# Optimization experiments

Measured on AMD Instinct MI355X. Metric: run time of the kernel, lower is better.

Reference implementation:

```python
import jax, jax.numpy as jnp
import numpy as np


def _gru_step(x, h, W_ih, W_hh, b_ih, b_hh):
    # torch GRUCell math, gate order (r, z, n)
    gx = x @ W_ih.T + b_ih
    gh = h @ W_hh.T + b_hh
    xr, xz, xn = jnp.split(gx, 3, axis=-1)
    hr, hz, hn = jnp.split(gh, 3, axis=-1)
    r = jax.nn.sigmoid(xr + hr)
    z = jax.nn.sigmoid(xz + hz)
    n = jnp.tanh(xn + r * hn)
    return (1.0 - z) * n + z * h


def setup_inputs() -> dict:
    T, B, S, E, H, Dv, EXT = 64, 16, 400, 128, 256, 50000, 50
    key = jax.random.key(0)
    ks = jax.random.split(key, 32)
    def rn(k, shape, s=0.05):
        return jax.random.normal(k, shape, dtype=jnp.float32) * s
    return {
        'embedded_y': rn(ks[0], (T, B, E), 1.0),
        'encode_outputs': rn(ks[1], (S, B, 2 * H), 1.0),
        'init_state': rn(ks[2], (B, H), 1.0),
        'x_mask': jnp.ones((S, B, 1), jnp.float32),
        'y_mask': jnp.ones((T, B, 1), jnp.float32),
        'x_index': jax.random.randint(ks[3], (S, B), 0, Dv + EXT),
        'max_ext_len': EXT,
        'init_coverage': jnp.zeros((B, S), jnp.float32),
        'W_h': rn(ks[4], (2 * H, 2 * H)),
        'W_s': rn(ks[5], (2 * H, H)),
        'W_c': rn(ks[6], (2 * H, 1)),
        'b_attn': rn(ks[7], (2 * H,)),
        'V_attn': rn(ks[8], (1, 2 * H)),
        'gru1_Wih': rn(ks[9], (3 * H, E)),
        'gru1_Whh': rn(ks[10], (3 * H, H)),
        'gru1_bih': rn(ks[11], (3 * H,)),
        'gru1_bhh': rn(ks[12], (3 * H,)),
        'gru2_Wih': rn(ks[13], (3 * H, 2 * H)),
        'gru2_Whh': rn(ks[14], (3 * H, H)),
        'gru2_bih': rn(ks[15], (3 * H,)),
        'gru2_bhh': rn(ks[16], (3 * H,)),
        'V1_w': rn(ks[17], (H, H + 2 * H + E)),
        'V1_b': rn(ks[18], (H,)),
        'V2_w': rn(ks[19], (Dv, H)),
        'V2_b': rn(ks[20], (Dv,)),
        'Wp_w': rn(ks[21], (1, H + 2 * H + E)),
        'Wp_b': rn(ks[22], (1,)),
    }


def reference(embedded_y, encode_outputs, init_state, x_mask, y_mask, x_index,
              max_ext_len, init_coverage, W_h, W_s, W_c, b_attn, V_attn,
              gru1_Wih, gru1_Whh, gru1_bih, gru1_bhh,
              gru2_Wih, gru2_Whh, gru2_bih, gru2_bhh,
              V1_w, V1_b, V2_w, V2_b, Wp_w, Wp_b):
    T, B, E = embedded_y.shape
    S = encode_outputs.shape[0]
    enc_proj = encode_outputs @ W_h.T  # [S,B,2H], time-invariant part of attention

    def step(carry, inp):
        hidden, cov = carry  # [B,H], [B,S]
        y_t, ym_t = inp      # [B,E], [B,1]
        s1 = _gru_step(y_t, hidden, gru1_Wih, gru1_Whh, gru1_bih, gru1_bhh)
        s1 = ym_t * s1 + (1.0 - ym_t) * hidden
        # coverage term: cov.T[:,:,None] is [S,B,1], Linear(1,2H)
        att = enc_proj + s1 @ W_s.T + cov.T[:, :, None] @ W_c.T + b_attn  # [S,B,2H]
        score = (jnp.tanh(att) * x_mask) @ V_attn.T                      # [S,B,1]
        score = jnp.where(x_mask == 0, -1e9, score)
        attn = jax.nn.softmax(score, axis=0)                             # over source len
        ctx = jnp.sum(attn * encode_outputs, axis=0)                     # [B,2H]
        s2 = _gru_step(ctx, s1, gru2_Wih, gru2_Whh, gru2_bih, gru2_bhh)
        s2 = ym_t * s2 + (1.0 - ym_t) * s1
        waw = attn[:, :, 0].T                                            # [B,S]
        return (s2, cov + waw), (s2, ctx, waw, cov)

    (_, _), (hs, cvs, waws, covs) = jax.lax.scan(
        step, (init_state, init_coverage), (embedded_y, y_mask))

    # WordProbLayer (pointer-generator)
    h = jnp.concatenate([hs, cvs, embedded_y], axis=2)         # [T,B,H+2H+E]
    logit = jnp.tanh(h @ V1_w.T + V1_b) @ V2_w.T + V2_b        # [T,B,Dv]
    y_dec = jax.nn.softmax(logit, axis=2)
    y_dec = jnp.concatenate(
        [y_dec, jnp.zeros((T, B, max_ext_len), y_dec.dtype)], axis=2)
    g = jax.nn.sigmoid(h @ Wp_w.T + Wp_b)                      # [T,B,1]
    xids = jnp.broadcast_to(x_index.T[None], (T, B, S))        # [T,B,S]
    ti = jnp.arange(T)[:, None, None]
    bi = jnp.arange(B)[None, :, None]
    y_pred = (g * y_dec).at[ti, bi, xids].add((1.0 - g) * waws)
    return (y_pred, hs, waws, covs)
```

## Files before the change

kernel.cpp:

```cpp
#include <hip/hip_runtime.h>
#include <hip/hip_bf16.h>

typedef unsigned short ushort_t;
typedef unsigned int u32;
typedef _Float16 f16;
typedef __attribute__((ext_vector_type(8))) short short8;
typedef __attribute__((ext_vector_type(4))) float f32x4;
typedef __attribute__((ext_vector_type(8))) _Float16 f16x8;
typedef __attribute__((ext_vector_type(4))) unsigned int u32x4;

#define T_ 64
#define B_ 16
#define S_ 400
#define E_ 128
#define H_ 256
#define H2_ 512
#define DV_ 50000
#define VOC_ 50050
#define CAT_ 896
#define NCLUS 8
#define RSL 50

#define YP_SZ   ((size_t)T_*B_*VOC_)
#define HS_OFF  (YP_SZ)
#define WW_OFF  (HS_OFF + (size_t)T_*B_*H_)
#define CV_OFF  (WW_OFF + (size_t)T_*B_*S_)
#define ENCP16_OFF ((size_t)0)
#define ENC16_OFF  ((size_t)1638400)
#define WS16_OFF   ((size_t)3276800)
#define W216_OFF   ((size_t)3342336)
#define CTXALL_OFF ((size_t)3538944)
#define GX1_OFF    ((size_t)4063232)
#define WH216_OFF  ((size_t)4947968)
#define WH116T_OFF ((size_t)5046272)
#define SYNC_OFF   ((size_t)5144576)
#define S1STR      528
#define S1TAG      520
#define S2STR      816
#define S2TAG      808
#define S2REG      ((size_t)16*NCLUS*S1STR)
#define SYNC_FLOATS ((size_t)16*NCLUS*(S1STR + S2STR))

#define WS_ROWSUM 0
#define WS_GV     1024
#define WS_G1     2048

__device__ __forceinline__ float fsig(float x){ return 1.f/(1.f+__expf(-x)); }
__device__ __forceinline__ float ftanh(float x){ float e=__expf(2.f*x); return 1.f - 2.f/(e+1.f); }

#define PADK(k) ((k) + (((k)>>5)<<2))

#define AT_ST(p, v)  __hip_atomic_store((p), (v), __ATOMIC_RELAXED, __HIP_MEMORY_SCOPE_AGENT)
#define AT_LD(p)     __hip_atomic_load((p), __ATOMIC_RELAXED, __HIP_MEMORY_SCOPE_AGENT)
#define AT_STI(p, v) __hip_atomic_store((int*)(p), (v), __ATOMIC_RELAXED, __HIP_MEMORY_SCOPE_AGENT)
#define AT_LDI(p)    __hip_atomic_load((const int*)(p), __ATOMIC_RELAXED, __HIP_MEMORY_SCOPE_AGENT)

#define SM_ENC    0
#define SM_ENCP   51200
#define SM_GH1    102400
#define SM_SWS    105472
#define SM_VP     107776
#define SM_WCP    110080
#define SM_UCTX   112384
#define SM_HID    114432
#define SM_S1     115456
#define SM_G2X    116480
#define SM_G2H    116864
#define SM_COV    117248
#define SM_EV     117504
#define SM_XM     117760
#define SM_YM     118016
#define SM_HIDH   118272
#define SM_S1H    118784
#define SM_CTXH   119296
#define SM_S2S    120320
#define SM_PART   120448
#define SM_B1     120512
#define SM_B2     123584
#define SM_B3     126656
#define SM_BYTES  129728

__global__ __launch_bounds__(256)
void cvt16_kernel(const float* src, f16* dst, int n){
  int i = blockIdx.x*256 + threadIdx.x;
  if (i < n) dst[i] = (f16)src[i];
}

__global__ __launch_bounds__(256)
void repack_kernel(const float* enc, f16* enc16){
  int s = blockIdx.x, b = blockIdx.y;
  const float* src = enc + ((size_t)s*B_ + b)*H2_;
  f16* dst = enc16 + ((size_t)b*S_ + s)*H2_;
  for (int k = threadIdx.x; k < H2_; k += 256) dst[k] = (f16)src[k];
}

__global__ __launch_bounds__(256)
void packWhh1_kernel(const float* W, f16* dst){
  int r = blockIdx.x, c = threadIdx.x;
  int jq = c >> 5, cc = c & 31;
  dst[((size_t)jq*768 + r)*32 + cc] = (f16)W[(size_t)r*H_ + c];
}

__global__ __launch_bounds__(256)
void gx1_kernel(const float* emb, const float* Wih1, const float* bih1, float* dout){
  __shared__ float As[64][33];
  __shared__ float Bs[128][33];
  int m0 = blockIdx.x*64, n0 = blockIdx.y*128;
  int tx = threadIdx.x & 15, ty = threadIdx.x >> 4;
  float acc[4][8] = {};
  for (int kt = 0; kt < E_; kt += 32){
    for (int l = threadIdx.x; l < 64*32; l += 256){
      int m = l>>5, k = l&31; As[m][k] = emb[(size_t)(m0+m)*E_ + kt + k];
    }
    for (int l = threadIdx.x; l < 128*32; l += 256){
      int n = l>>5, k = l&31; Bs[n][k] = Wih1[(size_t)(n0+n)*E_ + kt + k];
    }
    __syncthreads();
    for (int k = 0; k < 32; ++k){
      float a[4], bv[8];
      #pragma unroll
      for (int i=0;i<4;++i) a[i] = As[ty+16*i][k];
      #pragma unroll
      for (int j=0;j<8;++j) bv[j] = Bs[tx+16*j][k];
      #pragma unroll
      for (int i=0;i<4;++i)
        #pragma unroll
        for (int j=0;j<8;++j) acc[i][j] += a[i]*bv[j];
    }
    __syncthreads();
  }
  #pragma unroll
  for (int i=0;i<4;++i)
    #pragma unroll
    for (int j=0;j<8;++j){
      int m = m0 + ty + 16*i, n = n0 + tx + 16*j;
      dout[GX1_OFF + (size_t)m*768 + n] = acc[i][j] + bih1[n];
    }
}

__global__ __launch_bounds__(256)
void encproj_kernel(const float* enc, const float* Wh, const float* battn, float* dout){
  __shared__ float As[64][33];
  __shared__ float Bs[128][33];
  int m0 = blockIdx.x*64, n0 = blockIdx.y*128;
  int tx = threadIdx.x & 15, ty = threadIdx.x >> 4;
  float acc[4][8] = {};
  for (int kt = 0; kt < H2_; kt += 32){
    for (int l = threadIdx.x; l < 64*32; l += 256){
      int m = l>>5, k = l&31; As[m][k] = enc[(size_t)(m0+m)*H2_ + kt + k];
    }
    for (int l = threadIdx.x; l < 128*32; l += 256){
      int n = l>>5, k = l&31; Bs[n][k] = Wh[(size_t)(n0+n)*H2_ + kt + k];
    }
    __syncthreads();
    for (int k = 0; k < 32; ++k){
      float a[4], bv[8];
      #pragma unroll
      for (int i=0;i<4;++i) a[i] = As[ty+16*i][k];
      #pragma unroll
      for (int j=0;j<8;++j) bv[j] = Bs[tx+16*j][k];
      #pragma unroll
      for (int i=0;i<4;++i)
        #pragma unroll
        for (int j=0;j<8;++j) acc[i][j] += a[i]*bv[j];
    }
    __syncthreads();
  }
  f16* ep16 = (f16*)(dout + ENCP16_OFF);
  #pragma unroll
  for (int i=0;i<4;++i)
    #pragma unroll
    for (int j=0;j<8;++j){
      int m = m0 + ty + 16*i, n = n0 + tx + 16*j;
      int s = m >> 4, bb = m & 15;
      ep16[((size_t)bb*S_ + s)*H2_ + n] = (f16)(acc[i][j] + battn[n]);
    }
}

template<int R, int K, bool PAD>
__device__ __forceinline__ void gemv_f16t(const f16* W, const f16* xh, float* out_l, int tid){
  int o = tid >> 3, l8 = tid & 7;
  constexpr int NI = K/64;
  const f16x8* x8 = (const f16x8*)xh;
  f16x8 xv[NI];
  #pragma unroll
  for (int i = 0; i < NI; ++i) xv[i] = x8[i*8 + l8];
  #pragma unroll
  for (int it = 0; it < R/128; ++it){
    int d = o + it*128;
    const f16x8* w8 = (const f16x8*)(W + (size_t)d*K);
    float acc = 0.f;
    #pragma unroll
    for (int i = 0; i < NI; ++i){
      f16x8 w = w8[i*8 + l8];
      #pragma unroll
      for (int e = 0; e < 8; ++e) acc += (float)w[e] * (float)xv[i][e];
    }
    acc += __shfl_xor(acc,1,8); acc += __shfl_xor(acc,2,8); acc += __shfl_xor(acc,4,8);
    if (l8 == 0) out_l[PAD ? PADK(d) : d] = acc;
  }
}

__device__ __forceinline__ void spin_tags(const float* base, int stride, int tagoff, int want, int tid){
  if (tid < 64){
    bool mine = tid < NCLUS;
    const float* tp = base + (size_t)(mine ? tid : 0)*stride + tagoff;
    while (true){
      int v = mine ? AT_LDI(tp) : want;
      if (__all(v == want)) break;
      __builtin_amdgcn_s_sleep(1);
    }
  }
  __syncthreads();
}

__global__ __launch_bounds__(1024)
void scan_kernel(const float* xm, const float* ym,
                 const float* bhh1, const float* bih2, const float* bhh2,
                 const float* Wc, const float* Vat,
                 const float* inith, const float* initc,
                 float* dout)
{
  extern __shared__ char smem[];
  f16*   enc_s  = (f16*)(smem + SM_ENC);
  f16*   encp_s = (f16*)(smem + SM_ENCP);
  float* gh1_l  = (float*)(smem + SM_GH1);
  float* sWs_p  = (float*)(smem + SM_SWS);
  float* Vp     = (float*)(smem + SM_VP);
  float* Wcp    = (float*)(smem + SM_WCP);
  float* uctx   = (float*)(smem + SM_UCTX);
  float* hid_l  = (float*)(smem + SM_HID);
  float* s1_l   = (float*)(smem + SM_S1);
  float* g2x_l  = (float*)(smem + SM_G2X);
  float* g2h_l  = (float*)(smem + SM_G2H);
  float* cov_l  = (float*)(smem + SM_COV);
  float* ev_l   = (float*)(smem + SM_EV);
  float* xm_l   = (float*)(smem + SM_XM);
  float* ym_l   = (float*)(smem + SM_YM);
  f16*   hidh   = (f16*)(smem + SM_HIDH);
  f16*   s1h    = (f16*)(smem + SM_S1H);
  f16*   ctxh   = (f16*)(smem + SM_CTXH);
  float* s2s    = (float*)(smem + SM_S2S);
  float* part_l = (float*)(smem + SM_PART);
  float* b1l    = (float*)(smem + SM_B1);
  float* b2l    = (float*)(smem + SM_B2);
  float* b3l    = (float*)(smem + SM_B3);

  const f16* Ws16   = (const f16*)(dout + WS16_OFF);
  const f16* W216   = (const f16*)(dout + W216_OFF);
  const f16* Wh216  = (const f16*)(dout + WH216_OFF);
  const f16* Wh116T = (const f16*)(dout + WH116T_OFF);
  const float* gx1  = dout + GX1_OFF;

  int blk = blockIdx.x, tid = threadIdx.x;
  int b = blk & 15, jj = blk >> 4;
  int wv = tid >> 6, ln = tid & 63;

  float* sl1 = dout + SYNC_OFF + (size_t)b*NCLUS*S1STR;
  float* sl2 = dout + SYNC_OFF + S2REG + (size_t)b*NCLUS*S2STR;
  float* sl1my = sl1 + (size_t)jj*S1STR;
  float* sl2my = sl2 + (size_t)jj*S2STR;

  {
    const u32x4* encg  = (const u32x4*)(dout + ENC16_OFF)  + (size_t)b*25600 + jj*3200;
    const u32x4* encpg = (const u32x4*)(dout + ENCP16_OFF) + (size_t)b*25600 + jj*3200;
    u32x4* encs4  = (u32x4*)enc_s;
    u32x4* encps4 = (u32x4*)encp_s;
    for (int i = tid; i < 3200; i += 1024){ encs4[i] = encg[i]; encps4[i] = encpg[i]; }
  }
  if (tid < 32)  s2s[tid] = inith[b*H_ + jj*32 + tid];
  if (tid < 512){ Vp[PADK(tid)] = Vat[tid]; Wcp[PADK(tid)] = Wc[tid]; }
  if (tid < RSL){ int s = jj*RSL + tid; cov_l[tid] = initc[b*S_ + s]; xm_l[tid] = xm[(size_t)s*B_ + b]; }
  if (tid >= 512 && tid < 576) ym_l[tid-512] = ym[(tid-512)*B_ + b];
  if (tid < 768){ b1l[tid] = bhh1[tid]; b2l[tid] = bih2[tid]; b3l[tid] = bhh2[tid]; }
  __syncthreads();
  if (tid < 768){
    const f16x8* p8 = (const f16x8*)(Wh116T + ((size_t)jj*768 + tid)*32);
    float acc = 0.f;
    #pragma unroll
    for (int c4 = 0; c4 < 4; ++c4){
      f16x8 w = p8[c4];
      #pragma unroll
      for (int e = 0; e < 8; ++e) acc += (float)w[e] * s2s[c4*8+e];
    }
    AT_ST(&sl2my[tid], acc);
  } else if (tid < 800){
    AT_ST(&sl2my[768 + (tid-768)], s2s[tid-768]);
  }
  __syncthreads();
  if (tid == 0) AT_STI(&sl2my[S2TAG], 1);

  for (int t = 0; t < T_; ++t){
    int row = t*B_ + b;
    int want = t + 1;
    spin_tags(sl2, S2STR, S2TAG, want, tid);
    if (tid < 768){
      float a = 0.f;
      #pragma unroll
      for (int q = 0; q < NCLUS; ++q) a += AT_LD(&sl2[(size_t)q*S2STR + tid]);
      gh1_l[tid] = a;
    } else {
      int j = tid - 768;
      float h = AT_LD(&sl2[(size_t)(j>>5)*S2STR + 768 + (j&31)]);
      hid_l[j] = h; hidh[j] = (f16)h;
    }
    __syncthreads();
    if (tid < 256){
      int j = tid;
      const float* gx = gx1 + (size_t)row*768;
      float r = fsig(gx[j]      + gh1_l[j]      + b1l[j]);
      float z = fsig(gx[256+j]  + gh1_l[256+j]  + b1l[256+j]);
      float n = ftanh(gx[512+j] + r*(gh1_l[512+j] + b1l[512+j]));
      float h = hid_l[j];
      float ymv = ym_l[t];
      float s1 = ymv*((1.f-z)*n + z*h) + (1.f-ymv)*h;
      s1_l[j] = s1; s1h[j] = (f16)s1;
    }
    __syncthreads();
    gemv_f16t<512,256,true>(Ws16, s1h, sWs_p, tid);
    __syncthreads();
    {
      int kp = PADK(ln*8);
      float4 sA = *(const float4*)&sWs_p[kp], sB = *(const float4*)&sWs_p[kp+4];
      float4 vA = *(const float4*)&Vp[kp],    vB = *(const float4*)&Vp[kp+4];
      float4 cA = *(const float4*)&Wcp[kp],   cB = *(const float4*)&Wcp[kp+4];
      const f16x8* eps = (const f16x8*)encp_s;
      #pragma unroll
      for (int i = 0; i < 4; ++i){
        int r = wv + 16*i;
        if (r < RSL){
          f16x8 eu = eps[r*64 + ln];
          float cv = cov_l[r];
          float sc = 0.f;
          sc += ftanh((float)eu[0] + sA.x + cv*cA.x)*vA.x;
          sc += ftanh((float)eu[1] + sA.y + cv*cA.y)*vA.y;
          sc += ftanh((float)eu[2] + sA.z + cv*cA.z)*vA.z;
          sc += ftanh((float)eu[3] + sA.w + cv*cA.w)*vA.w;
          sc += ftanh((float)eu[4] + sB.x + cv*cB.x)*vB.x;
          sc += ftanh((float)eu[5] + sB.y + cv*cB.y)*vB.y;
          sc += ftanh((float)eu[6] + sB.z + cv*cB.z)*vB.z;
          sc += ftanh((float)eu[7] + sB.w + cv*cB.w)*vB.w;
          sc += __shfl_xor(sc,1);  sc += __shfl_xor(sc,2);  sc += __shfl_xor(sc,4);
          sc += __shfl_xor(sc,8);  sc += __shfl_xor(sc,16); sc += __shfl_xor(sc,32);
          if (ln == 0){
            float xmv = xm_l[r];
            ev_l[r] = __expf((xmv == 0.f) ? -1e9f : xmv*sc);
          }
        }
      }
    }
    __syncthreads();
    if (tid < 512){
      float acc = 0.f;
      #pragma unroll 5
      for (int s = 0; s < RSL; ++s) acc += ev_l[s] * (float)enc_s[s*H2_ + tid];
      AT_ST(&sl1my[tid], acc);
    } else if (tid >= 960){
      int l = tid - 960;
      float v = (l < RSL) ? ev_l[l] : 0.f;
      v += __shfl_xor(v,1);  v += __shfl_xor(v,2);  v += __shfl_xor(v,4);
      v += __shfl_xor(v,8);  v += __shfl_xor(v,16); v += __shfl_xor(v,32);
      if (l == 0) AT_ST(&sl1my[512], v);
    }
    __syncthreads();
    if (tid == 0) AT_STI(&sl1my[S1TAG], want);
    {
      int o = tid >> 3, l8 = tid & 7;
      if (o < 96){
        int g = o >> 5, m = o & 31, wrow = g*256 + jj*32 + m;
        const f16x8* w8 = (const f16x8*)(Wh216 + (size_t)wrow*H_);
        const f16x8* x8 = (const f16x8*)s1h;
        float acc = 0.f;
        #pragma unroll
        for (int i = 0; i < 4; ++i){
          f16x8 w = w8[i*8 + l8], x = x8[i*8 + l8];
          #pragma unroll
          for (int e = 0; e < 8; ++e) acc += (float)w[e] * (float)x[e];
        }
        acc += __shfl_xor(acc,1,8); acc += __shfl_xor(acc,2,8); acc += __shfl_xor(acc,4,8);
        if (l8 == 0) g2h_l[o] = acc;
      }
    }
    spin_tags(sl1, S1STR, S1TAG, want, tid);
    if (tid < 512){
      float us = 0.f;
      #pragma unroll
      for (int q = 0; q < NCLUS; ++q) us += AT_LD(&sl1[(size_t)q*S1STR + tid]);
      uctx[tid] = us;
    } else if (tid < 512 + NCLUS){
      part_l[tid-512] = AT_LD(&sl1[(size_t)(tid-512)*S1STR + 512]);
    }
    __syncthreads();
    {
      float es = 0.f;
      #pragma unroll
      for (int q = 0; q < NCLUS; ++q) es += part_l[q];
      float inv = 1.f/es;
      if (tid < 512){
        float v = uctx[tid]*inv;
        ctxh[tid] = (f16)v;
        if (jj == 0) __builtin_nontemporal_store(v, &dout[CTXALL_OFF + (size_t)row*H2_ + tid]);
      } else if (tid >= 640 && tid < 640 + RSL){
        int r = tid - 640;
        float w_ = ev_l[r]*inv;
        size_t ro = (size_t)row*S_ + jj*RSL + r;
        __builtin_nontemporal_store(w_, &dout[WW_OFF + ro]);
        float co = cov_l[r];
        __builtin_nontemporal_store(co, &dout[CV_OFF + ro]);
        cov_l[r] = co + w_;
      }
    }
    __syncthreads();
    {
      int o = tid >> 3, l8 = tid & 7;
      if (o < 96){
        int g = o >> 5, m = o & 31, wrow = g*256 + jj*32 + m;
        const f16x8* w8 = (const f16x8*)(W216 + (size_t)wrow*H2_);
        const f16x8* x8 = (const f16x8*)ctxh;
        float acc = 0.f;
        #pragma unroll
        for (int i = 0; i < 8; ++i){
          f16x8 w = w8[i*8 + l8], x = x8[i*8 + l8];
          #pragma unroll
          for (int e = 0; e < 8; ++e) acc += (float)w[e] * (float)x[e];
        }
        acc += __shfl_xor(acc,1,8); acc += __shfl_xor(acc,2,8); acc += __shfl_xor(acc,4,8);
        if (l8 == 0) g2x_l[o] = acc;
      }
    }
    __syncthreads();
    if (tid < 32){
      int i = tid, j = jj*32 + i;
      float r = fsig(g2x_l[i]     + b2l[j]     + g2h_l[i]    + b3l[j]);
      float z = fsig(g2x_l[32+i]  + b2l[256+j] + g2h_l[32+i] + b3l[256+j]);
      float n = ftanh(g2x_l[64+i] + b2l[512+j] + r*(g2h_l[64+i] + b3l[512+j]));
      float s1v = s1_l[j];
      float ymv = ym_l[t];
      float s2 = ymv*((1.f-z)*n + z*s1v) + (1.f-ymv)*s1v;
      s2s[i] = s2;
      AT_ST(&sl2my[768 + i], s2);
      __builtin_nontemporal_store(s2, &dout[HS_OFF + (size_t)row*H_ + j]);
    }
    __syncthreads();
    if (tid < 768){
      const f16x8* p8 = (const f16x8*)(Wh116T + ((size_t)jj*768 + tid)*32);
      float acc = 0.f;
      #pragma unroll
      for (int c4 = 0; c4 < 4; ++c4){
        f16x8 w = p8[c4];
        #pragma unroll
        for (int e = 0; e < 8; ++e) acc += (float)w[e] * s2s[c4*8+e];
      }
      AT_ST(&sl2my[tid], acc);
    }
    __syncthreads();
    if (tid == 0) AT_STI(&sl2my[S2TAG], t + 2);
  }
}

__global__ __launch_bounds__(512)
void head_kernel(const float* emb, const float* V1w, const float* V1b,
                 const float* Wpw, const float* Wpb, float* dout, float* ws)
{
  __shared__ float hc[2][CAT_];
  int t = blockIdx.x, b0 = blockIdx.y*2, tid = threadIdx.x;
  for (int i = tid; i < 2*CAT_; i += 512){
    int bb = i / CAT_, k = i % CAT_;
    int b = b0 + bb;
    float v;
    if (k < H_)           v = dout[HS_OFF     + ((size_t)(t*B_+b))*H_  + k];
    else if (k < H_+H2_)  v = dout[CTXALL_OFF + ((size_t)(t*B_+b))*H2_ + (k-H_)];
    else                  v = emb[((size_t)(t*B_+b))*E_ + (k-H_-H2_)];
    hc[bb][k] = v;
  }
  __syncthreads();
  __hip_bfloat16* G1 = (__hip_bfloat16*)(ws + WS_G1);
  {
    int j = tid & 255, bb = tid >> 8;
    const float* wv = V1w + (size_t)j*CAT_;
    float acc = 0.f;
    #pragma unroll 8
    for (int k = 0; k < CAT_; ++k) acc += hc[bb][k]*wv[k];
    G1[((size_t)(t*B_ + b0 + bb))*H_ + j] = __float2bfloat16(ftanh(acc + V1b[j]));
  }
  if (tid < 128){
    int bb = tid >> 6, l = tid & 63;
    float acc = 0.f;
    for (int k = l; k < CAT_; k += 64) acc += hc[bb][k]*Wpw[k];
    acc += __shfl_xor(acc,1);  acc += __shfl_xor(acc,2);  acc += __shfl_xor(acc,4);
    acc += __shfl_xor(acc,8);  acc += __shfl_xor(acc,16); acc += __shfl_xor(acc,32);
    if (l == 0) ws[WS_GV + t*B_ + b0 + bb] = fsig(acc + Wpb[0]);
  }
}

__global__ __launch_bounds__(256)
void gemm2_kernel(const ushort_t* G1, const float* V2w, const float* V2b,
                  float* dout, float* rowsum)
{
  __shared__ float rows_l[128];
  int tid = threadIdx.x;
  if (tid < 128) rows_l[tid] = 0.f;
  int m0 = blockIdx.y * 128;
  int n0 = blockIdx.x * 64;
  int lane = tid & 63, w = tid >> 6;
  int c16 = lane & 15, kg = lane >> 4;
  int col = n0 + w*16 + c16;
  int colc = col < DV_ ? col : DV_-1;
  bool valid = col < DV_;
  f32x4 acc[8] = {};
  const float* brow = V2w + (size_t)colc*H_;
  for (int ks = 0; ks < 8; ++ks){
    int k0 = ks*32 + kg*8;
    short8 bf;
    #pragma unroll
    for (int i = 0; i < 8; ++i){
      __hip_bfloat16 hb = __float2bfloat16(brow[k0+i]);
      union { __hip_bfloat16 h; short s; } u; u.h = hb;
      bf[i] = u.s;
    }
    #pragma unroll
    for (int mf = 0; mf < 8; ++mf){
      const short8* ap = (const short8*)(G1 + ((size_t)(m0 + mf*16 + c16))*H_ + k0);
      acc[mf] = __builtin_amdgcn_mfma_f32_16x16x32_bf16(*ap, bf, acc[mf], 0, 0, 0);
    }
  }
  float bias = valid ? V2b[colc] : 0.f;
  __syncthreads();
  #pragma unroll
  for (int mf = 0; mf < 8; ++mf){
    #pragma unroll
    for (int r = 0; r < 4; ++r){
      float v = valid ? __expf(acc[mf][r] + bias) : 0.f;
      int rloc = mf*16 + kg*4 + r;
      if (valid) dout[(size_t)(m0 + rloc)*VOC_ + col] = v;
      float s = v;
      s += __shfl_xor(s, 1, 16); s += __shfl_xor(s, 2, 16);
      s += __shfl_xor(s, 4, 16); s += __shfl_xor(s, 8, 16);
      if (c16 == 0) atomicAdd(&rows_l[rloc], s);
    }
  }
  __syncthreads();
  if (tid < 128) atomicAdd(&rowsum[m0 + tid], rows_l[tid]);
}

__global__ __launch_bounds__(256)
void norm_kernel(float* dout, const float* ws){
  int row = blockIdx.x;
  float sc = ws[WS_GV + row] / ws[WS_ROWSUM + row];
  float2* y2 = (float2*)(dout + (size_t)row * VOC_);
  for (int i = threadIdx.x; i < VOC_/2; i += 256){
    float2 v = y2[i];
    int e0 = 2*i;
    v.x = (e0   < DV_) ? v.x*sc : 0.f;
    v.y = (e0+1 < DV_) ? v.y*sc : 0.f;
    y2[i] = v;
  }
}

__global__ __launch_bounds__(256)
void scatter_kernel(float* dout, const float* ws, const int* xidx){
  int row = blockIdx.x; int b = row & 15;
  float g1 = 1.f - ws[WS_GV + row];
  const float* ww = dout + WW_OFF + (size_t)row*S_;
  float* y = dout + (size_t)row*VOC_;
  for (int s = threadIdx.x; s < S_; s += 256){
    atomicAdd(&y[xidx[(size_t)s*B_ + b]], g1*ww[s]);
  }
}

extern "C" void kernel_launch(void* const* d_in, const int* in_sizes, int n_in,
                              void* d_out, int out_size, void* d_ws, size_t ws_size,
                              hipStream_t stream)
{
  (void)in_sizes; (void)n_in; (void)out_size; (void)ws_size;
  const float* emb   = (const float*)d_in[0];
  const float* enc   = (const float*)d_in[1];
  const float* inith = (const float*)d_in[2];
  const float* xmask = (const float*)d_in[3];
  const float* ymask = (const float*)d_in[4];
  const int*   xidx  = (const int*)d_in[5];
  const float* initc = (const float*)d_in[7];
  const float* Wh    = (const float*)d_in[8];
  const float* Wss   = (const float*)d_in[9];
  const float* Wc    = (const float*)d_in[10];
  const float* battn = (const float*)d_in[11];
  const float* Vat   = (const float*)d_in[12];
  const float* Wih1  = (const float*)d_in[13];
  const float* Whh1  = (const float*)d_in[14];
  const float* bih1  = (const float*)d_in[15];
  const float* bhh1  = (const float*)d_in[16];
  const float* Wih2  = (const float*)d_in[17];
  const float* Whh2  = (const float*)d_in[18];
  const float* bih2  = (const float*)d_in[19];
  const float* bhh2  = (const float*)d_in[20];
  const float* V1w   = (const float*)d_in[21];
  const float* V1b   = (const float*)d_in[22];
  const float* V2w   = (const float*)d_in[23];
  const float* V2b   = (const float*)d_in[24];
  const float* Wpw   = (const float*)d_in[25];
  const float* Wpb   = (const float*)d_in[26];
  float* out = (float*)d_out;
  float* ws  = (float*)d_ws;

  hipFuncSetAttribute(reinterpret_cast<const void*>(scan_kernel),
                      hipFuncAttributeMaxDynamicSharedMemorySize, SM_BYTES);

  hipMemsetAsync(d_ws, 0, 2048*sizeof(float), stream);
  hipMemsetAsync(out + SYNC_OFF, 0, SYNC_FLOATS*sizeof(float), stream);
  cvt16_kernel<<<512,  256, 0, stream>>>(Wss,  (f16*)(out + WS16_OFF), H2_*H_);
  cvt16_kernel<<<1536, 256, 0, stream>>>(Wih2, (f16*)(out + W216_OFF), 3*H_*H2_);
  cvt16_kernel<<<768,  256, 0, stream>>>(Whh2, (f16*)(out + WH216_OFF), 3*H_*H_);
  packWhh1_kernel<<<768, 256, 0, stream>>>(Whh1, (f16*)(out + WH116T_OFF));
  repack_kernel<<<dim3(S_, B_), 256, 0, stream>>>(enc, (f16*)(out + ENC16_OFF));
  gx1_kernel<<<dim3(16, 6), 256, 0, stream>>>(emb, Wih1, bih1, out);
  encproj_kernel<<<dim3(100, 4), 256, 0, stream>>>(enc, Wh, battn, out);
  scan_kernel<<<128, 1024, SM_BYTES, stream>>>(xmask, ymask,
      bhh1, bih2, bhh2, Wc, Vat, inith, initc, out);
  head_kernel<<<dim3(T_, 8), 512, 0, stream>>>(emb, V1w, V1b, Wpw, Wpb, out, ws);
  gemm2_kernel<<<dim3(782, 8), 256, 0, stream>>>((const ushort_t*)(ws + WS_G1), V2w, V2b, out, ws + WS_ROWSUM);
  norm_kernel<<<1024, 256, 0, stream>>>(out, ws);
  scatter_kernel<<<1024, 256, 0, stream>>>(out, ws, xidx);
}
```

Before: 2.108 ms.

## Use MFMA for encoder projection, fp16 head weights, and fuse norm and scatter

The scalar fp32 encoder-projection GEMM is replaced by an MFMA fp16 kernel that reads the already-converted fp16 encoder copy and a newly converted fp16 W_h. V1 weights are converted to fp16 so the head GEMV reads half the bytes. Inside the scan kernel, the Whh1 slice is held in registers, the next step's gx1 row is prefetched into shared memory, and one shared-memory reduction stage plus its barrier is removed by summing the sync slots directly. The norm and scatter kernels are merged into one launch. The changes add two conversion launches and lower the precision of the encoder projection and V1 products.

```diff
diff --git a/kernel.cpp b/kernel.cpp
--- a/kernel.cpp
+++ b/kernel.cpp
@@ -40,6 +40,8 @@
 #define S2TAG      808
 #define S2REG      ((size_t)16*NCLUS*S1STR)
 #define SYNC_FLOATS ((size_t)16*NCLUS*(S1STR + S2STR))
+#define WH16F_OFF  ((size_t)5316608)
+#define V1HF_OFF   ((size_t)5447680)
 
 #define WS_ROWSUM 0
 #define WS_GV     1024
@@ -74,11 +76,11 @@
 #define SM_S1H    118784
 #define SM_CTXH   119296
 #define SM_S2S    120320
-#define SM_PART   120448
 #define SM_B1     120512
 #define SM_B2     123584
 #define SM_B3     126656
-#define SM_BYTES  129728
+#define SM_GX     129728
+#define SM_BYTES  132800
 
 __global__ __launch_bounds__(256)
 void cvt16_kernel(const float* src, f16* dst, int n){
@@ -139,41 +141,37 @@
 }
 
 __global__ __launch_bounds__(256)
-void encproj_kernel(const float* enc, const float* Wh, const float* battn, float* dout){
-  __shared__ float As[64][33];
-  __shared__ float Bs[128][33];
-  int m0 = blockIdx.x*64, n0 = blockIdx.y*128;
-  int tx = threadIdx.x & 15, ty = threadIdx.x >> 4;
-  float acc[4][8] = {};
-  for (int kt = 0; kt < H2_; kt += 32){
-    for (int l = threadIdx.x; l < 64*32; l += 256){
-      int m = l>>5, k = l&31; As[m][k] = enc[(size_t)(m0+m)*H2_ + kt + k];
-    }
-    for (int l = threadIdx.x; l < 128*32; l += 256){
-      int n = l>>5, k = l&31; Bs[n][k] = Wh[(size_t)(n0+n)*H2_ + kt + k];
-    }
-    __syncthreads();
-    for (int k = 0; k < 32; ++k){
-      float a[4], bv[8];
-      #pragma unroll
-      for (int i=0;i<4;++i) a[i] = As[ty+16*i][k];
-      #pragma unroll
-      for (int j=0;j<8;++j) bv[j] = Bs[tx+16*j][k];
-      #pragma unroll
-      for (int i=0;i<4;++i)
-        #pragma unroll
-        for (int j=0;j<8;++j) acc[i][j] += a[i]*bv[j];
-    }
-    __syncthreads();
-  }
-  f16* ep16 = (f16*)(dout + ENCP16_OFF);
+void encproj_mfma(const f16* enc16, const f16* Wh16, const float* battn, f16* ep16){
+  int nx = blockIdx.x, my = blockIdx.y, bz = blockIdx.z;
+  int tid = threadIdx.x;
+  int w = tid >> 6, lane = tid & 63;
+  int c16 = lane & 15, kg = lane >> 4;
+  int m0 = my*64, n0 = nx*128 + w*32;
+  f32x4 acc[4][2] = {};
+  int col0 = n0 + c16, col1 = n0 + 16 + c16;
+  for (int ks = 0; ks < 16; ++ks){
+    int k0 = ks*32 + kg*8;
+    f16x8 b0 = *(const f16x8*)(Wh16 + (size_t)col0*H2_ + k0);
+    f16x8 b1 = *(const f16x8*)(Wh16 + (size_t)col1*H2_ + k0);
+    #pragma unroll
+    for (int mf = 0; mf < 4; ++mf){
+      int s = m0 + mf*16 + c16; if (s > S_-1) s = S_-1;
+      f16x8 a = *(const f16x8*)(enc16 + ((size_t)bz*S_ + s)*H2_ + k0);
+      acc[mf][0] = __builtin_amdgcn_mfma_f32_16x16x32_f16(a, b0, acc[mf][0], 0, 0, 0);
+      acc[mf][1] = __builtin_amdgcn_mfma_f32_16x16x32_f16(a, b1, acc[mf][1], 0, 0, 0);
+    }
+  }
   #pragma unroll
-  for (int i=0;i<4;++i)
-    #pragma unroll
-    for (int j=0;j<8;++j){
-      int m = m0 + ty + 16*i, n = n0 + tx + 16*j;
-      int s = m >> 4, bb = m & 15;
-      ep16[((size_t)bb*S_ + s)*H2_ + n] = (f16)(acc[i][j] + battn[n]);
+  for (int mf = 0; mf < 4; ++mf)
+    #pragma unroll
+    for (int nf = 0; nf < 2; ++nf){
+      int col = n0 + nf*16 + c16;
+      float bb = battn[col];
+      #pragma unroll
+      for (int r = 0; r < 4; ++r){
+        int s = m0 + mf*16 + kg*4 + r;
+        if (s < S_) ep16[((size_t)bz*S_ + s)*H2_ + col] = (f16)(acc[mf][nf][r] + bb);
+      }
     }
 }
 
@@ -228,7 +226,6 @@
   float* sWs_p  = (float*)(smem + SM_SWS);
   float* Vp     = (float*)(smem + SM_VP);
   float* Wcp    = (float*)(smem + SM_WCP);
-  float* uctx   = (float*)(smem + SM_UCTX);
   float* hid_l  = (float*)(smem + SM_HID);
   float* s1_l   = (float*)(smem + SM_S1);
   float* g2x_l  = (float*)(smem + SM_G2X);
@@ -241,10 +238,10 @@
   f16*   s1h    = (f16*)(smem + SM_S1H);
   f16*   ctxh   = (f16*)(smem + SM_CTXH);
   float* s2s    = (float*)(smem + SM_S2S);
-  float* part_l = (float*)(smem + SM_PART);
   float* b1l    = (float*)(smem + SM_B1);
   float* b2l    = (float*)(smem + SM_B2);
   float* b3l    = (float*)(smem + SM_B3);
+  float* gxbuf  = (float*)(smem + SM_GX);
 
   const f16* Ws16   = (const f16*)(dout + WS16_OFF);
   const f16* W216   = (const f16*)(dout + W216_OFF);
@@ -260,6 +257,12 @@
   float* sl2 = dout + SYNC_OFF + S2REG + (size_t)b*NCLUS*S2STR;
   float* sl1my = sl1 + (size_t)jj*S1STR;
   float* sl2my = sl2 + (size_t)jj*S2STR;
+
+  f16x8 wh1r0, wh1r1, wh1r2, wh1r3;
+  if (tid < 768){
+    const f16x8* p8 = (const f16x8*)(Wh116T + ((size_t)jj*768 + tid)*32);
+    wh1r0 = p8[0]; wh1r1 = p8[1]; wh1r2 = p8[2]; wh1r3 = p8[3];
+  }
 
   {
     const u32x4* encg  = (const u32x4*)(dout + ENC16_OFF)  + (size_t)b*25600 + jj*3200;
@@ -272,17 +275,19 @@
   if (tid < 512){ Vp[PADK(tid)] = Vat[tid]; Wcp[PADK(tid)] = Wc[tid]; }
   if (tid < RSL){ int s = jj*RSL + tid; cov_l[tid] = initc[b*S_ + s]; xm_l[tid] = xm[(size_t)s*B_ + b]; }
   if (tid >= 512 && tid < 576) ym_l[tid-512] = ym[(tid-512)*B_ + b];
-  if (tid < 768){ b1l[tid] = bhh1[tid]; b2l[tid] = bih2[tid]; b3l[tid] = bhh2[tid]; }
+  if (tid < 768){ b1l[tid] = bhh1[tid]; b2l[tid] = bih2[tid]; b3l[tid] = bhh2[tid];
+                  gxbuf[tid] = gx1[(size_t)b*768 + tid]; }
   __syncthreads();
   if (tid < 768){
-    const f16x8* p8 = (const f16x8*)(Wh116T + ((size_t)jj*768 + tid)*32);
     float acc = 0.f;
     #pragma unroll
-    for (int c4 = 0; c4 < 4; ++c4){
-      f16x8 w = p8[c4];
-      #pragma unroll
-      for (int e = 0; e < 8; ++e) acc += (float)w[e] * s2s[c4*8+e];
-    }
+    for (int e = 0; e < 8; ++e) acc += (float)wh1r0[e]*s2s[e];
+    #pragma unroll
+    for (int e = 0; e < 8; ++e) acc += (float)wh1r1[e]*s2s[8+e];
+    #pragma unroll
+    for (int e = 0; e < 8; ++e) acc += (float)wh1r2[e]*s2s[16+e];
+    #pragma unroll
+    for (int e = 0; e < 8; ++e) acc += (float)wh1r3[e]*s2s[24+e];
     AT_ST(&sl2my[tid], acc);
   } else if (tid < 800){
     AT_ST(&sl2my[768 + (tid-768)], s2s[tid-768]);
@@ -307,10 +312,9 @@
     __syncthreads();
     if (tid < 256){
       int j = tid;
-      const float* gx = gx1 + (size_t)row*768;
-      float r = fsig(gx[j]      + gh1_l[j]      + b1l[j]);
-      float z = fsig(gx[256+j]  + gh1_l[256+j]  + b1l[256+j]);
-      float n = ftanh(gx[512+j] + r*(gh1_l[512+j] + b1l[512+j]));
+      float r = fsig(gxbuf[j]      + gh1_l[j]      + b1l[j]);
+      float z = fsig(gxbuf[256+j]  + gh1_l[256+j]  + b1l[256+j]);
+      float n = ftanh(gxbuf[512+j] + r*(gh1_l[512+j] + b1l[512+j]));
       float h = hid_l[j];
       float ymv = ym_l[t];
       float s1 = ymv*((1.f-z)*n + z*h) + (1.f-ymv)*h;
@@ -364,6 +368,11 @@
     }
     __syncthreads();
     if (tid == 0) AT_STI(&sl1my[S1TAG], want);
+    float gxn = 0.f;
+    if (tid < 768){
+      int tn = (t+1 < T_) ? t+1 : t;
+      gxn = gx1[(size_t)(tn*B_ + b)*768 + tid];
+    }
     {
       int o = tid >> 3, l8 = tid & 7;
       if (o < 96){
@@ -381,23 +390,18 @@
         if (l8 == 0) g2h_l[o] = acc;
       }
     }
+    if (tid < 768) gxbuf[tid] = gxn;
     spin_tags(sl1, S1STR, S1TAG, want, tid);
-    if (tid < 512){
-      float us = 0.f;
-      #pragma unroll
-      for (int q = 0; q < NCLUS; ++q) us += AT_LD(&sl1[(size_t)q*S1STR + tid]);
-      uctx[tid] = us;
-    } else if (tid < 512 + NCLUS){
-      part_l[tid-512] = AT_LD(&sl1[(size_t)(tid-512)*S1STR + 512]);
-    }
-    __syncthreads();
     {
       float es = 0.f;
       #pragma unroll
-      for (int q = 0; q < NCLUS; ++q) es += part_l[q];
+      for (int q = 0; q < NCLUS; ++q) es += AT_LD(&sl1[(size_t)q*S1STR + 512]);
       float inv = 1.f/es;
       if (tid < 512){
-        float v = uctx[tid]*inv;
+        float us = 0.f;
+        #pragma unroll
+        for (int q = 0; q < NCLUS; ++q) us += AT_LD(&sl1[(size_t)q*S1STR + tid]);
+        float v = us*inv;
         ctxh[tid] = (f16)v;
         if (jj == 0) __builtin_nontemporal_store(v, &dout[CTXALL_OFF + (size_t)row*H2_ + tid]);
       } else if (tid >= 640 && tid < 640 + RSL){
@@ -443,14 +447,15 @@
     }
     __syncthreads();
     if (tid < 768){
-      const f16x8* p8 = (const f16x8*)(Wh116T + ((size_t)jj*768 + tid)*32);
       float acc = 0.f;
       #pragma unroll
-      for (int c4 = 0; c4 < 4; ++c4){
-        f16x8 w = p8[c4];
-        #pragma unroll
-        for (int e = 0; e < 8; ++e) acc += (float)w[e] * s2s[c4*8+e];
-      }
+      for (int e = 0; e < 8; ++e) acc += (float)wh1r0[e]*s2s[e];
+      #pragma unroll
+      for (int e = 0; e < 8; ++e) acc += (float)wh1r1[e]*s2s[8+e];
+      #pragma unroll
+      for (int e = 0; e < 8; ++e) acc += (float)wh1r2[e]*s2s[16+e];
+      #pragma unroll
+      for (int e = 0; e < 8; ++e) acc += (float)wh1r3[e]*s2s[24+e];
       AT_ST(&sl2my[tid], acc);
     }
     __syncthreads();
@@ -459,7 +464,7 @@
 }
 
 __global__ __launch_bounds__(512)
-void head_kernel(const float* emb, const float* V1w, const float* V1b,
+void head_kernel(const float* emb, const f16* V1H, const float* V1b,
                  const float* Wpw, const float* Wpb, float* dout, float* ws)
 {
   __shared__ float hc[2][CAT_];
@@ -477,10 +482,14 @@
   __hip_bfloat16* G1 = (__hip_bfloat16*)(ws + WS_G1);
   {
     int j = tid & 255, bb = tid >> 8;
-    const float* wv = V1w + (size_t)j*CAT_;
+    const f16x8* wv8 = (const f16x8*)(V1H + (size_t)j*CAT_);
     float acc = 0.f;
-    #pragma unroll 8
-    for (int k = 0; k < CAT_; ++k) acc += hc[bb][k]*wv[k];
+    #pragma unroll 4
+    for (int kk = 0; kk < CAT_/8; ++kk){
+      f16x8 w = wv8[kk];
+      #pragma unroll
+      for (int e = 0; e < 8; ++e) acc += hc[bb][kk*8+e]*(float)w[e];
+    }
     G1[((size_t)(t*B_ + b0 + bb))*H_ + j] = __float2bfloat16(ftanh(acc + V1b[j]));
   }
   if (tid < 128){
@@ -544,9 +553,11 @@
 }
 
 __global__ __launch_bounds__(256)
-void norm_kernel(float* dout, const float* ws){
-  int row = blockIdx.x;
-  float sc = ws[WS_GV + row] / ws[WS_ROWSUM + row];
+void normscatter_kernel(float* dout, const float* ws, const int* xidx){
+  int row = blockIdx.x; int b = row & 15;
+  float gv = ws[WS_GV + row];
+  float sc = gv / ws[WS_ROWSUM + row];
+  float g1 = 1.f - gv;
   float2* y2 = (float2*)(dout + (size_t)row * VOC_);
   for (int i = threadIdx.x; i < VOC_/2; i += 256){
     float2 v = y2[i];
@@ -555,12 +566,7 @@
     v.y = (e0+1 < DV_) ? v.y*sc : 0.f;
     y2[i] = v;
   }
-}
-
-__global__ __launch_bounds__(256)
-void scatter_kernel(float* dout, const float* ws, const int* xidx){
-  int row = blockIdx.x; int b = row & 15;
-  float g1 = 1.f - ws[WS_GV + row];
+  __syncthreads();
   const float* ww = dout + WW_OFF + (size_t)row*S_;
   float* y = dout + (size_t)row*VOC_;
   for (int s = threadIdx.x; s < S_; s += 256){
@@ -610,14 +616,17 @@
   cvt16_kernel<<<512,  256, 0, stream>>>(Wss,  (f16*)(out + WS16_OFF), H2_*H_);
   cvt16_kernel<<<1536, 256, 0, stream>>>(Wih2, (f16*)(out + W216_OFF), 3*H_*H2_);
   cvt16_kernel<<<768,  256, 0, stream>>>(Whh2, (f16*)(out + WH216_OFF), 3*H_*H_);
+  cvt16_kernel<<<1024, 256, 0, stream>>>(Wh,   (f16*)(out + WH16F_OFF), H2_*H2_);
+  cvt16_kernel<<<896,  256, 0, stream>>>(V1w,  (f16*)(out + V1HF_OFF), H_*CAT_);
   packWhh1_kernel<<<768, 256, 0, stream>>>(Whh1, (f16*)(out + WH116T_OFF));
   repack_kernel<<<dim3(S_, B_), 256, 0, stream>>>(enc, (f16*)(out + ENC16_OFF));
   gx1_kernel<<<dim3(16, 6), 256, 0, stream>>>(emb, Wih1, bih1, out);
-  encproj_kernel<<<dim3(100, 4), 256, 0, stream>>>(enc, Wh, battn, out);
+  encproj_mfma<<<dim3(4, 7, B_), 256, 0, stream>>>((const f16*)(out + ENC16_OFF),
+      (const f16*)(out + WH16F_OFF), battn, (f16*)(out + ENCP16_OFF));
   scan_kernel<<<128, 1024, SM_BYTES, stream>>>(xmask, ymask,
       bhh1, bih2, bhh2, Wc, Vat, inith, initc, out);
-  head_kernel<<<dim3(T_, 8), 512, 0, stream>>>(emb, V1w, V1b, Wpw, Wpb, out, ws);
+  head_kernel<<<dim3(T_, 8), 512, 0, stream>>>(emb, (const f16*)(out + V1HF_OFF),
+      V1b, Wpw, Wpb, out, ws);
   gemm2_kernel<<<dim3(782, 8), 256, 0, stream>>>((const ushort_t*)(ws + WS_G1), V2w, V2b, out, ws + WS_ROWSUM);
-  norm_kernel<<<1024, 256, 0, stream>>>(out, ws);
-  scatter_kernel<<<1024, 256, 0, stream>>>(out, ws, xidx);
-}
+  normscatter_kernel<<<1024, 256, 0, stream>>>(out, ws, xidx);
+}
```

Result: slower. 2.383 ms (+13.1%).
